# Kernel tuning notes

Measured on AMD Instinct MI355X. Metric: run time of the kernel, lower is better.

Reference implementation:

```python
import jax, jax.numpy as jnp
import numpy as np

N = 100000   # nodes
E = 1600000  # edges
H = 150      # hidden_dim
G = 256      # num graphs in batch
L = 5        # num_layers
GATE_H = 200


def setup_inputs() -> dict:
    key = jax.random.key(0)
    ks = jax.random.split(key, 12)
    s = lambda k, shape, fan: jax.random.normal(k, shape, dtype=jnp.float32) / np.sqrt(fan)
    return {
        "x": jax.random.normal(ks[0], (N, H), dtype=jnp.float32),
        "edge_index": jax.random.randint(ks[1], (2, E), 0, N, dtype=jnp.int64),
        "batch": jnp.sort(jax.random.randint(ks[2], (N,), 0, G, dtype=jnp.int64)),
        "W": s(ks[3], (L, H, H), H),              # GatedGraphConv per-layer weight
        "w_ih": s(ks[4], (3 * H, H), H),           # GRUCell input weights (r,z,n)
        "w_hh": s(ks[5], (3 * H, H), H),
        "b_ih": jnp.zeros((3 * H,), jnp.float32),
        "b_hh": jnp.zeros((3 * H,), jnp.float32),
        "gw1": s(ks[6], (H, GATE_H), H),           # gate_nn Linear(150,200)
        "gb1": jnp.zeros((GATE_H,), jnp.float32),
        "gw2": s(ks[7], (GATE_H, 1), GATE_H),      # gate_nn Linear(200,1)
        "gb2": jnp.zeros((1,), jnp.float32),
    }


def _gru_cell(m, h, w_ih, w_hh, b_ih, b_hh):
    gi = m @ w_ih.T + b_ih   # [N, 3H]
    gh = h @ w_hh.T + b_hh
    ir, iz, inn = jnp.split(gi, 3, axis=-1)
    hr, hz, hn = jnp.split(gh, 3, axis=-1)
    r = jax.nn.sigmoid(ir + hr)
    z = jax.nn.sigmoid(iz + hz)
    n = jnp.tanh(inn + r * hn)
    return (1.0 - z) * n + z * h


def reference(x, edge_index, batch, W, w_ih, w_hh, b_ih, b_hh, gw1, gb1, gw2, gb2):
    src, dst = edge_index[0], edge_index[1]
    h = x
    # GatedGraphConv: per layer, linear transform, scatter_add aggregation, GRU update
    for i in range(L):
        m = h @ W[i]                                   # [N, H]
        agg = jax.ops.segment_sum(m[src], dst, num_segments=N)  # scatter_add over edges
        h = _gru_cell(agg, h, w_ih, w_hh, b_ih, b_hh)
    # GlobalAttention readout
    gate = jnp.tanh(h @ gw1 + gb1) @ gw2 + gb2          # [N, 1]
    gmax = jax.ops.segment_max(gate, batch, num_segments=G)    # [G, 1]
    gate = jnp.exp(gate - gmax[batch])
    gsum = jax.ops.segment_sum(gate, batch, num_segments=G)    # [G, 1]
    gate = gate / (gsum[batch] + 1e-16)                 # segment softmax
    out = jax.ops.segment_sum(gate * h, batch, num_segments=G)  # [G, H]
    return out, gate
```

## Files before the change

kernel.cpp:

```cpp
#include <hip/hip_runtime.h>
#include <math.h>

#define NN 100000
#define NE 1600000
#define H 150
#define NG 256
#define NL 5
#define GH 200
#define HS 160
#define LS 168
#define CHN 1563
#define CH2 782
#define SNB 98
#define CSRMAX 2304000
#define NB 196
#define EBLK 782

typedef unsigned short u16;
typedef unsigned int   u32;
typedef __attribute__((ext_vector_type(8))) short bf16x8;
typedef __attribute__((ext_vector_type(4))) float f32x4;

__device__ __forceinline__ float bf2f(u32 lo16){ u32 t = lo16 << 16; return __builtin_bit_cast(float, t); }
__device__ __forceinline__ u16 f2bf(float f){
  u32 u = __builtin_bit_cast(u32, f);
  u += 0x7fffu + ((u >> 16) & 1u);
  return (u16)(u >> 16);
}
__device__ __forceinline__ u32 pack2(float a, float b){ return (u32)f2bf(a) | ((u32)f2bf(b) << 16); }
__device__ __forceinline__ float fast_sig(float x){
  float e = __expf(-x);
  return __builtin_amdgcn_rcpf(1.f + e);
}
__device__ __forceinline__ float fast_tanh(float x){
  float cx = fminf(fmaxf(x, -15.f), 15.f);
  float e = __expf(2.f*cx);
  return (e - 1.f) * __builtin_amdgcn_rcpf(e + 1.f);
}

__global__ void k_hist(const int* __restrict__ ed, int* __restrict__ cnt){
  int e = blockIdx.x*256 + threadIdx.x;
  if (e < NE) atomicAdd(&cnt[ed[e]], 1);
}

__global__ __launch_bounds__(256) void k_scan1(const int* __restrict__ cnt, int* __restrict__ part){
  __shared__ int red[256];
  const int b = blockIdx.x, tid = threadIdx.x;
  const int base = b*1024;
  int s = 0;
  #pragma unroll
  for (int i = 0; i < 4; ++i){
    int idx = base + tid + i*256;
    int v = (idx < NN) ? cnt[idx] : 0;
    s += (v + 7) & ~7;
  }
  red[tid] = s; __syncthreads();
  for (int st = 128; st >= 1; st >>= 1){
    if (tid < st) red[tid] += red[tid+st];
    __syncthreads();
  }
  if (tid == 0) part[b] = red[0];
}

__global__ void k_scan2(int* __restrict__ part){
  const int t = threadIdx.x;
  int v0 = (2*t   < SNB) ? part[2*t]   : 0;
  int v1 = (2*t+1 < SNB) ? part[2*t+1] : 0;
  int s = v0 + v1, x = s;
  #pragma unroll
  for (int off = 1; off < 64; off <<= 1){
    int tt = __shfl_up(x, off);
    if (t >= off) x += tt;
  }
  int excl = x - s;
  if (2*t   < SNB) part[2*t]   = excl;
  if (2*t+1 < SNB) part[2*t+1] = excl + v0;
}

__global__ __launch_bounds__(1024) void k_scan3(const int* __restrict__ cnt,
        const int* __restrict__ part, int* __restrict__ rowptr, int* __restrict__ cursor){
  __shared__ int wsum[16];
  const int b = blockIdx.x, tid = threadIdx.x;
  const int wid = tid >> 6, lane = tid & 63;
  const int idx = b*1024 + tid;
  int c = (idx < NN) ? cnt[idx] : 0;
  int v = (c + 7) & ~7;
  int x = v;
  #pragma unroll
  for (int off = 1; off < 64; off <<= 1){
    int t = __shfl_up(x, off);
    if (lane >= off) x += t;
  }
  if (lane == 63) wsum[wid] = x;
  __syncthreads();
  if (tid < 16){
    int s = wsum[tid];
    int y = s;
    #pragma unroll
    for (int off = 1; off < 16; off <<= 1){
      int t = __shfl_up(y, off);
      if (tid >= off) y += t;
    }
    wsum[tid] = y - s;
  }
  __syncthreads();
  if (idx < NN){
    int incl = part[b] + wsum[wid] + x;
    rowptr[idx+1] = incl;
    cursor[idx]   = incl - v;
  }
  if (idx == 0) rowptr[0] = 0;
}

__global__ __launch_bounds__(256) void k_pre(int* __restrict__ csr){
  int i = (blockIdx.x*256 + threadIdx.x)*4;
  int4 v = {NN, NN, NN, NN};
  *(int4*)&csr[i] = v;
}

__global__ __launch_bounds__(256) void k_bhist(const int* __restrict__ ed, int* __restrict__ bcnt){
  __shared__ int bh[NB];
  const int tid = threadIdx.x;
  for (int i = tid; i < NB; i += 256) bh[i] = 0;
  __syncthreads();
  const int base = blockIdx.x*2048;
  #pragma unroll
  for (int i = 0; i < 8; ++i){
    int e = base + i*256 + tid;
    if (e < NE) atomicAdd(&bh[ed[e] >> 9], 1);
  }
  __syncthreads();
  for (int i = tid; i < NB; i += 256) if (bh[i]) atomicAdd(&bcnt[i], bh[i]);
}

__global__ void k_bscan(const int* __restrict__ bcnt, int* __restrict__ bcur){
  __shared__ int ws[4];
  const int t = threadIdx.x, lane = t & 63, w = t >> 6;
  int v = (t < NB) ? bcnt[t] : 0;
  int x = v;
  #pragma unroll
  for (int off = 1; off < 64; off <<= 1){
    int tt = __shfl_up(x, off);
    if (lane >= off) x += tt;
  }
  if (lane == 63) ws[w] = x;
  __syncthreads();
  if (t == 0){
    int s = 0;
    #pragma unroll
    for (int i = 0; i < 4; ++i){ int tmp = ws[i]; ws[i] = s; s += tmp; }
  }
  __syncthreads();
  if (t < NB) bcur[t] = ws[w] + x - v;
}

__global__ __launch_bounds__(256) void k_bscatter(const int* __restrict__ es,
        const int* __restrict__ ed, int* __restrict__ bcur, int2* __restrict__ ebuf){
  __shared__ int lh[NB];
  __shared__ int lbase[NB];
  const int tid = threadIdx.x;
  for (int i = tid; i < NB; i += 256) lh[i] = 0;
  __syncthreads();
  const int base = blockIdx.x*2048;
  u32 meta[8]; int srcs[8], dsts[8];
  #pragma unroll
  for (int i = 0; i < 8; ++i){
    int e = base + i*256 + tid;
    if (e < NE){
      int d = ed[e];
      int b = d >> 9;
      int lr = atomicAdd(&lh[b], 1);
      meta[i] = ((u32)b << 16) | (u32)lr;
      srcs[i] = es[e]; dsts[i] = d;
    } else meta[i] = 0xffffffffu;
  }
  __syncthreads();
  for (int i = tid; i < NB; i += 256){
    int c = lh[i];
    lbase[i] = c ? atomicAdd(&bcur[i], c) : 0;
  }
  __syncthreads();
  #pragma unroll
  for (int i = 0; i < 8; ++i){
    if (meta[i] != 0xffffffffu){
      int b = meta[i] >> 16, lr = meta[i] & 0xffff;
      ebuf[lbase[b] + lr] = make_int2(srcs[i], dsts[i]);
    }
  }
}

__global__ void k_fill2(const int2* __restrict__ ebuf, int* __restrict__ cursor,
                        int* __restrict__ csr){
  int e = blockIdx.x*256 + threadIdx.x;
  if (e < NE){
    int2 sd = ebuf[e];
    int pos = atomicAdd(&cursor[sd.y], 1);
    csr[pos] = sd.x;
  }
}

__global__ __launch_bounds__(256) void k_wc(const float* __restrict__ W,
        const float* __restrict__ wih, float* __restrict__ Wc){
  int idx = blockIdx.x*256 + threadIdx.x;
  if (idx >= NL*H*450) return;
  int l = idx / (H*450);
  int rem = idx - l*H*450;
  int k = rem / 450;
  int j = rem - k*450;
  const float* Wr = W   + (size_t)l*H*H + (size_t)k*H;
  const float* wr = wih + (size_t)j*H;
  float acc = 0.f;
  for (int t = 0; t < H; ++t) acc = fmaf(Wr[t], wr[t], acc);
  Wc[idx] = acc;
}

__global__ void k_packi(const float* __restrict__ Wc, short* __restrict__ wbi){
  int idx = blockIdx.x*256 + threadIdx.x;
  int li = idx & 511;
  int q = idx >> 9;
  int mat = q % 3; q /= 3;
  int ks = q % 5;  q /= 5;
  int ct = q % 10; int l = q / 10;
  int lane = li >> 3, j = li & 7;
  int k = ks*32 + ((lane >> 4) << 3) + j;
  int col = ct*16 + (lane & 15);
  float v = (k < H && col < H) ? Wc[(size_t)l*H*450 + (size_t)k*450 + mat*H + col] : 0.f;
  wbi[idx] = (short)f2bf(v);
}

__global__ void k_packh(const float* __restrict__ whh, short* __restrict__ wbh){
  int idx = blockIdx.x*256 + threadIdx.x;
  int li = idx & 511;
  int q = idx >> 9;
  int mat = q % 3; q /= 3;
  int ks = q % 5;  int ct = q / 5;
  int lane = li >> 3, j = li & 7;
  int k = ks*32 + ((lane >> 4) << 3) + j;
  int col = ct*16 + (lane & 15);
  float v = (k < H && col < H) ? whh[(size_t)(mat*H + col)*H + k] : 0.f;
  wbh[idx] = (short)f2bf(v);
}

__global__ void k_packg(const float* __restrict__ gw1, short* __restrict__ gw1b){
  int idx = blockIdx.x*256 + threadIdx.x;
  int li = idx & 511;
  int q = idx >> 9;
  int ks = q % 5;  int ct = q / 5;
  int lane = li >> 3, j = li & 7;
  int k = ks*32 + ((lane >> 4) << 3) + j;
  int col = ct*16 + (lane & 15);
  float v = (k < H && col < GH) ? gw1[(size_t)k*GH + col] : 0.f;
  gw1b[idx] = (short)f2bf(v);
}

__global__ void k_cvt(const float* __restrict__ x, short* __restrict__ hb){
  int idx = blockIdx.x*256 + threadIdx.x;
  if (idx >= NN*80) return;
  int n = idx / 80, c2 = idx - n*80;
  int c = c2*2;
  float lo = (c   < H) ? x[(size_t)n*H + c]   : 0.f;
  float hi = (c+1 < H) ? x[(size_t)n*H + c+1] : 0.f;
  ((u32*)hb)[idx] = (u32)f2bf(lo) | ((u32)f2bf(hi) << 16);
}

__global__ void k_zrow(short* __restrict__ a, short* __restrict__ b){
  int t = threadIdx.x;
  if (t < 80){
    ((u32*)a)[(size_t)NN*80 + t] = 0u;
    ((u32*)b)[(size_t)NN*80 + t] = 0u;
  }
}

__global__ __launch_bounds__(256) void k_gather(const short* __restrict__ hb,
        const int* __restrict__ rowptr, const int* __restrict__ csr,
        short* __restrict__ aggb){
  const int lane = threadIdx.x & 63;
  const int n = blockIdx.x*4 + (threadIdx.x >> 6);
  if (n >= NN) return;
  const int s0 = rowptr[n], s1 = rowptr[n+1];
  const u32* h32 = (const u32*)hb;
  const bool ext = lane < 16;
  float x0=0.f, x1=0.f, y0=0.f, y1=0.f;
  for (int j = s0; j < s1; j += 8){
    int4 ia = *(const int4*)&csr[j];
    int4 ib = *(const int4*)&csr[j+4];
    const u32* r0 = h32 + (size_t)ia.x*80;
    const u32* r1 = h32 + (size_t)ia.y*80;
    const u32* r2 = h32 + (size_t)ia.z*80;
    const u32* r3 = h32 + (size_t)ia.w*80;
    const u32* r4 = h32 + (size_t)ib.x*80;
    const u32* r5 = h32 + (size_t)ib.y*80;
    const u32* r6 = h32 + (size_t)ib.z*80;
    const u32* r7 = h32 + (size_t)ib.w*80;
    u32 v0 = r0[lane], v1 = r1[lane], v2 = r2[lane], v3 = r3[lane];
    u32 v4 = r4[lane], v5 = r5[lane], v6 = r6[lane], v7 = r7[lane];
    u32 u0=0,u1=0,u2=0,u3=0,u4=0,u5=0,u6=0,u7=0;
    if (ext){
      u0 = r0[64+lane]; u1 = r1[64+lane]; u2 = r2[64+lane]; u3 = r3[64+lane];
      u4 = r4[64+lane]; u5 = r5[64+lane]; u6 = r6[64+lane]; u7 = r7[64+lane];
    }
    x0 += bf2f(v0 & 0xffffu) + bf2f(v1 & 0xffffu) + bf2f(v2 & 0xffffu) + bf2f(v3 & 0xffffu)
        + bf2f(v4 & 0xffffu) + bf2f(v5 & 0xffffu) + bf2f(v6 & 0xffffu) + bf2f(v7 & 0xffffu);
    x1 += bf2f(v0 >> 16) + bf2f(v1 >> 16) + bf2f(v2 >> 16) + bf2f(v3 >> 16)
        + bf2f(v4 >> 16) + bf2f(v5 >> 16) + bf2f(v6 >> 16) + bf2f(v7 >> 16);
    if (ext){
      y0 += bf2f(u0 & 0xffffu) + bf2f(u1 & 0xffffu) + bf2f(u2 & 0xffffu) + bf2f(u3 & 0xffffu)
          + bf2f(u4 & 0xffffu) + bf2f(u5 & 0xffffu) + bf2f(u6 & 0xffffu) + bf2f(u7 & 0xffffu);
      y1 += bf2f(u0 >> 16) + bf2f(u1 >> 16) + bf2f(u2 >> 16) + bf2f(u3 >> 16)
          + bf2f(u4 >> 16) + bf2f(u5 >> 16) + bf2f(u6 >> 16) + bf2f(u7 >> 16);
    }
  }
  u32* o = (u32*)aggb + (size_t)n*80;
  o[lane] = pack2(x0, x1);
  if (ext) o[64+lane] = pack2(y0, y1);
}

__global__ __launch_bounds__(256, 2) void k_gru(
    const short* __restrict__ aggb, const short* __restrict__ hbc,
    short* __restrict__ hbn,
    const short* __restrict__ wbi_l, const short* __restrict__ wbh,
    const float* __restrict__ bih, const float* __restrict__ bhh){
  __shared__ short sB[2][15360];
  const int tid = threadIdx.x;
  const int w = tid >> 6, lane = tid & 63;
  const int l16 = lane & 15, g = lane >> 4, g8 = g*8;
  const int row0 = blockIdx.x*128 + w*32;

  bf16x8 fA[2][5], fH[2][5];
  #pragma unroll
  for (int t = 0; t < 2; ++t){
    const int r = row0 + t*16 + l16;
    const bool rv = r < NN;
    #pragma unroll
    for (int ks = 0; ks < 5; ++ks){
      bf16x8 va = {0,0,0,0,0,0,0,0}, vh = {0,0,0,0,0,0,0,0};
      if (rv){
        va = *(const bf16x8*)&aggb[(size_t)r*HS + ks*32 + g8];
        vh = *(const bf16x8*)&hbc [(size_t)r*HS + ks*32 + g8];
      }
      fA[t][ks] = va; fH[t][ks] = vh;
    }
  }

  bf16x8 pr[8];
  #pragma unroll
  for (int k2 = 0; k2 < 8; ++k2){
    int u = tid + k2*256;
    if (u < 1920){
      int s = u >> 6, e = u & 63;
      const short* src = (s < 15) ? (wbi_l + s*512 + e*8)
                                  : (wbh  + (s-15)*512 + e*8);
      pr[k2] = *(const bf16x8*)src;
    }
  }
  #pragma unroll
  for (int k2 = 0; k2 < 8; ++k2){
    int u = tid + k2*256;
    if (u < 1920) *(bf16x8*)&sB[0][u*8] = pr[k2];
  }

  for (int ct = 0; ct < 10; ++ct){
    const int cur = ct & 1;
    __syncthreads();
    if (ct < 9){
      const int cto = (ct+1)*7680;
      #pragma unroll
      for (int k2 = 0; k2 < 8; ++k2){
        int u = tid + k2*256;
        if (u < 1920){
          int s = u >> 6, e = u & 63;
          const short* src = (s < 15) ? (wbi_l + cto + s*512 + e*8)
                                      : (wbh  + cto + (s-15)*512 + e*8);
          pr[k2] = *(const bf16x8*)src;
        }
      }
    }

    const int col = ct*16 + l16;
    const bool cv = col < H;
    const float bir = cv ? bih[col] : 0.f, biz = cv ? bih[H+col] : 0.f, bin_ = cv ? bih[2*H+col] : 0.f;
    const float bhr = cv ? bhh[col] : 0.f, bhz = cv ? bhh[H+col] : 0.f, bhn  = cv ? bhh[2*H+col] : 0.f;

    f32x4 ai[2][3], ah[2][3];
    #pragma unroll
    for (int t = 0; t < 2; ++t)
      #pragma unroll
      for (int m = 0; m < 3; ++m){ ai[t][m] = (f32x4){0,0,0,0}; ah[t][m] = (f32x4){0,0,0,0}; }

    const short* sbc = sB[cur];
    #pragma unroll
    for (int ks = 0; ks < 5; ++ks){
      bf16x8 bi0 = *(const bf16x8*)&sbc[(ks*3+0)*512 + lane*8];
      bf16x8 bi1 = *(const bf16x8*)&sbc[(ks*3+1)*512 + lane*8];
      bf16x8 bi2 = *(const bf16x8*)&sbc[(ks*3+2)*512 + lane*8];
      bf16x8 bh0 = *(const bf16x8*)&sbc[(15+ks*3+0)*512 + lane*8];
      bf16x8 bh1 = *(const bf16x8*)&sbc[(15+ks*3+1)*512 + lane*8];
      bf16x8 bh2 = *(const bf16x8*)&sbc[(15+ks*3+2)*512 + lane*8];
      #pragma unroll
      for (int t = 0; t < 2; ++t){
        ai[t][0] = __builtin_amdgcn_mfma_f32_16x16x32_bf16(fA[t][ks], bi0, ai[t][0], 0,0,0);
        ai[t][1] = __builtin_amdgcn_mfma_f32_16x16x32_bf16(fA[t][ks], bi1, ai[t][1], 0,0,0);
        ai[t][2] = __builtin_amdgcn_mfma_f32_16x16x32_bf16(fA[t][ks], bi2, ai[t][2], 0,0,0);
        ah[t][0] = __builtin_amdgcn_mfma_f32_16x16x32_bf16(fH[t][ks], bh0, ah[t][0], 0,0,0);
        ah[t][1] = __builtin_amdgcn_mfma_f32_16x16x32_bf16(fH[t][ks], bh1, ah[t][1], 0,0,0);
        ah[t][2] = __builtin_amdgcn_mfma_f32_16x16x32_bf16(fH[t][ks], bh2, ah[t][2], 0,0,0);
      }
    }

    if (ct < 9){
      #pragma unroll
      for (int k2 = 0; k2 < 8; ++k2){
        int u = tid + k2*256;
        if (u < 1920) *(bf16x8*)&sB[cur^1][u*8] = pr[k2];
      }
    }

    if (cv){
      #pragma unroll
      for (int t = 0; t < 2; ++t){
        #pragma unroll
        for (int r = 0; r < 4; ++r){
          int grow = row0 + t*16 + g*4 + r;
          if (grow < NN){
            float rr = fast_sig(ai[t][0][r]+bir + ah[t][0][r]+bhr);
            float zz = fast_sig(ai[t][1][r]+biz + ah[t][1][r]+bhz);
            float nn = fast_tanh(ai[t][2][r]+bin_ + rr*(ah[t][2][r]+bhn));
            float hold = bf2f((u32)(u16)hbc[(size_t)grow*HS + col]);
            float hnew = (1.f-zz)*nn + zz*hold;
            hbn[(size_t)grow*HS + col] = (short)f2bf(hnew);
          }
        }
      }
    }
  }
}

__global__ __launch_bounds__(256) void k_gatepre(const short* __restrict__ hb,
      const short* __restrict__ gw1b, const float* __restrict__ gb1,
      const float* __restrict__ gw2, const float* __restrict__ gb2,
      float* __restrict__ gbuf){
  __shared__ short sh[64*LS];
  __shared__ float part[4][4][4][4];
  const int tid = threadIdx.x;
  const int w = tid >> 6, lane = tid & 63;
  const int l16 = lane & 15, g = lane >> 4, g8 = g*8;
  const int chunk = blockIdx.x, row0 = chunk*64;

  for (int i = tid; i < 64*20; i += 256){
    int r = i/20, c = i - r*20;
    int gr = row0 + r;
    bf16x8 v = {0,0,0,0,0,0,0,0};
    if (gr < NN) v = *(const bf16x8*)&hb[(size_t)gr*HS + c*8];
    *(bf16x8*)&sh[r*LS + c*8] = v;
  }
  __syncthreads();

  float acc[4][4];
  #pragma unroll
  for (int rt=0; rt<4; ++rt){
    #pragma unroll
    for (int r=0; r<4; ++r) acc[rt][r] = 0.f;
  }
  for (int ct = w; ct < 13; ct += 4){
    bf16x8 B[5];
    const short* p = gw1b + (size_t)(ct*5)*512 + lane*8;
    #pragma unroll
    for (int ks = 0; ks < 5; ++ks) B[ks] = *(const bf16x8*)&p[ks*512];
    int col = ct*16 + l16;
    bool cv = col < GH;
    float g2 = cv ? gw2[col] : 0.f;
    float b1 = cv ? gb1[col] : 0.f;
    #pragma unroll
    for (int rt = 0; rt < 4; ++rt){
      f32x4 d = {0,0,0,0};
      #pragma unroll
      for (int ks = 0; ks < 5; ++ks){
        bf16x8 aH = *(const bf16x8*)&sh[(rt*16 + l16)*LS + ks*32 + g8];
        d = __builtin_amdgcn_mfma_f32_16x16x32_bf16(aH, B[ks], d, 0,0,0);
      }
      if (cv){
        #pragma unroll
        for (int r = 0; r < 4; ++r) acc[rt][r] += fast_tanh(d[r] + b1) * g2;
      }
    }
  }
  #pragma unroll
  for (int rt = 0; rt < 4; ++rt){
    #pragma unroll
    for (int r = 0; r < 4; ++r){
      float v = acc[rt][r];
      v += __shfl_xor(v, 1); v += __shfl_xor(v, 2);
      v += __shfl_xor(v, 4); v += __shfl_xor(v, 8);
      if (l16 == 0) part[w][rt][g][r] = v;
    }
  }
  __syncthreads();
  if (tid < 64){
    int rt = tid >> 4, gg = (tid >> 2) & 3, r = tid & 3;
    int grow = row0 + tid;
    if (grow < NN)
      gbuf[grow] = part[0][rt][gg][r] + part[1][rt][gg][r]
                 + part[2][rt][gg][r] + part[3][rt][gg][r] + gb2[0];
  }
}

__global__ __launch_bounds__(512) void k_readout(float* __restrict__ gatebuf,
    const short* __restrict__ hb, const int* __restrict__ batch,
    float* __restrict__ out, float* __restrict__ gate_out){
  const int g = blockIdx.x;
  const int tid = threadIdx.x;
  int lo=0, hi=NN;
  while (lo<hi){ int mid=(lo+hi)>>1; if (batch[mid] < g) lo=mid+1; else hi=mid; }
  const int start = lo;
  hi = NN;
  while (lo<hi){ int mid=(lo+hi)>>1; if (batch[mid] < g+1) lo=mid+1; else hi=mid; }
  const int end = lo;

  __shared__ float red[512];
  __shared__ float pacc[6][80][2];
  __shared__ float s_max, s_inv;
  float mx = -INFINITY;
  for (int n = start+tid; n < end; n += 512) mx = fmaxf(mx, gatebuf[n]);
  red[tid]=mx; __syncthreads();
  for (int s=256; s>=1; s>>=1){ if (tid<s) red[tid]=fmaxf(red[tid],red[tid+s]); __syncthreads(); }
  if (tid==0) s_max = red[0];
  __syncthreads();
  const float gmax = s_max;
  float sum = 0.f;
  for (int n = start+tid; n < end; n += 512){
    float e = expf(gatebuf[n]-gmax);
    gatebuf[n] = e;
    sum += e;
  }
  red[tid]=sum; __syncthreads();
  for (int s=256; s>=1; s>>=1){ if (tid<s) red[tid]+=red[tid+s]; __syncthreads(); }
  if (tid==0) s_inv = 1.0f/(red[0] + 1e-16f);
  __syncthreads();
  const float inv = s_inv;
  for (int n = start+tid; n < end; n += 512) gate_out[n] = gatebuf[n]*inv;

  const int col = tid % 80;
  const int grp = tid / 80;
  const u32* h32 = (const u32*)hb;
  if (grp < 6){
    float a0 = 0.f, a1 = 0.f;
    for (int n = start + grp; n < end; n += 6){
      u32 v = h32[(size_t)n*80 + col];
      float gv = gatebuf[n];
      a0 = fmaf(gv, bf2f(v & 0xffffu), a0);
      a1 = fmaf(gv, bf2f(v >> 16),     a1);
    }
    pacc[grp][col][0] = a0;
    pacc[grp][col][1] = a1;
  }
  __syncthreads();
  if (tid < 80){
    float a0 = 0.f, a1 = 0.f;
    #pragma unroll
    for (int q = 0; q < 6; ++q){ a0 += pacc[q][tid][0]; a1 += pacc[q][tid][1]; }
    int c0 = 2*tid, c1 = 2*tid + 1;
    if (c0 < H) out[g*H + c0] = a0*inv;
    if (c1 < H) out[g*H + c1] = a1*inv;
  }
}

extern "C" void kernel_launch(void* const* d_in, const int* in_sizes, int n_in,
                              void* d_out, int out_size, void* d_ws, size_t ws_size,
                              hipStream_t stream) {
  (void)in_sizes; (void)n_in; (void)out_size; (void)ws_size;
  const float* x    = (const float*)d_in[0];
  const int*   eidx = (const int*)d_in[1];
  const int*   batch= (const int*)d_in[2];
  const float* W    = (const float*)d_in[3];
  const float* wih  = (const float*)d_in[4];
  const float* whh  = (const float*)d_in[5];
  const float* bih  = (const float*)d_in[6];
  const float* bhh  = (const float*)d_in[7];
  const float* gw1  = (const float*)d_in[8];
  const float* gb1  = (const float*)d_in[9];
  const float* gw2  = (const float*)d_in[10];
  const float* gb2  = (const float*)d_in[11];

  float* out      = (float*)d_out;
  float* gate_out = out + NG*H;

  char* p = (char*)d_ws;
  float* gbuf  = (float*)p;  p += (size_t)NN*4;
  float* Wc    = (float*)p;  p += (size_t)NL*H*450*4;
  short* hb0   = (short*)p;  p += (size_t)(NN+1)*HS*2;
  short* hb1   = (short*)p;  p += (size_t)(NN+1)*HS*2;
  short* aggb  = (short*)p;  p += (size_t)NN*HS*2;
  short* wbi   = (short*)p;  p += (size_t)NL*76800*2;
  short* wbh   = (short*)p;  p += (size_t)76800*2;
  short* gw1b  = (short*)p;  p += (size_t)33280*2;
  int*   cnt   = (int*)p;    p += (size_t)NN*4;
  int*   rowptr= (int*)p;    p += (size_t)(NN+1)*4;
  int*   cursor= (int*)p;    p += (size_t)NN*4;
  int*   csr   = (int*)p;    p += (size_t)CSRMAX*4;
  int*   spart = (int*)p;    p += (size_t)SNB*4;
  int*   bcnt  = (int*)p;    p += (size_t)NB*4;
  int*   bcur  = (int*)p;    p += (size_t)NB*4;
  int2*  ebuf  = (int2*)p;   p += (size_t)NE*8;

  const int* esrc = eidx;
  const int* edst = eidx + NE;

  hipMemsetAsync(cnt, 0, sizeof(int)*NN, stream);
  hipMemsetAsync(bcnt, 0, sizeof(int)*NB, stream);
  k_hist<<<(NE+255)/256, 256, 0, stream>>>(edst, cnt);
  k_scan1<<<SNB, 256, 0, stream>>>(cnt, spart);
  k_scan2<<<1, 64, 0, stream>>>(spart);
  k_scan3<<<SNB, 1024, 0, stream>>>(cnt, spart, rowptr, cursor);
  k_pre <<<CSRMAX/1024, 256, 0, stream>>>(csr);
  k_bhist<<<EBLK, 256, 0, stream>>>(edst, bcnt);
  k_bscan<<<1, 256, 0, stream>>>(bcnt, bcur);
  k_bscatter<<<EBLK, 256, 0, stream>>>(esrc, edst, bcur, ebuf);
  k_fill2<<<(NE+255)/256, 256, 0, stream>>>(ebuf, cursor, csr);

  k_wc   <<<(NL*H*450+255)/256, 256, 0, stream>>>(W, wih, Wc);
  k_packi<<<1500, 256, 0, stream>>>(Wc, wbi);
  k_packh<<<300,  256, 0, stream>>>(whh, wbh);
  k_packg<<<130,  256, 0, stream>>>(gw1, gw1b);

  k_cvt<<<(NN*80+255)/256, 256, 0, stream>>>(x, hb0);
  k_zrow<<<1, 128, 0, stream>>>(hb0, hb1);

  for (int l = 0; l < NL; ++l){
    short* cur  = (l & 1) ? hb1 : hb0;
    short* next = (l & 1) ? hb0 : hb1;
    k_gather<<<NN/4, 256, 0, stream>>>(cur, rowptr, csr, aggb);
    k_gru<<<CH2, 256, 0, stream>>>(aggb, cur, next,
                                   wbi + (size_t)l*76800, wbh, bih, bhh);
  }
  k_gatepre<<<CHN, 256, 0, stream>>>(hb1, gw1b, gb1, gw2, gb2, gbuf);
  k_readout<<<NG, 512, 0, stream>>>(gbuf, hb1, batch, out, gate_out);
}
```

Before: 1.145 ms.

## Gather from column-sliced hidden-state copies so each block touches one slice

```diff
diff --git a/kernel.cpp b/kernel.cpp
--- a/kernel.cpp
+++ b/kernel.cpp
@@ -15,6 +15,7 @@
 #define CSRMAX 2304000
 #define NB 196
 #define EBLK 782
+#define SLICE_U32 1000010
 
 typedef unsigned short u16;
 typedef unsigned int   u32;
@@ -253,71 +254,67 @@
   gw1b[idx] = (short)f2bf(v);
 }
 
-__global__ void k_cvt(const float* __restrict__ x, short* __restrict__ hb){
+__global__ void k_cvt(const float* __restrict__ x, short* __restrict__ hb,
+                      u32* __restrict__ hbs){
   int idx = blockIdx.x*256 + threadIdx.x;
   if (idx >= NN*80) return;
   int n = idx / 80, c2 = idx - n*80;
   int c = c2*2;
   float lo = (c   < H) ? x[(size_t)n*H + c]   : 0.f;
   float hi = (c+1 < H) ? x[(size_t)n*H + c+1] : 0.f;
-  ((u32*)hb)[idx] = (u32)f2bf(lo) | ((u32)f2bf(hi) << 16);
-}
-
-__global__ void k_zrow(short* __restrict__ a, short* __restrict__ b){
+  u32 packed = (u32)f2bf(lo) | ((u32)f2bf(hi) << 16);
+  ((u32*)hb)[idx] = packed;
+  int cs = c2 / 10, off = c2 - cs*10;
+  hbs[(size_t)cs*SLICE_U32 + (size_t)n*10 + off] = packed;
+}
+
+__global__ void k_zrow(short* __restrict__ a, short* __restrict__ b,
+                       u32* __restrict__ sa, u32* __restrict__ sb){
   int t = threadIdx.x;
   if (t < 80){
     ((u32*)a)[(size_t)NN*80 + t] = 0u;
     ((u32*)b)[(size_t)NN*80 + t] = 0u;
-  }
-}
-
-__global__ __launch_bounds__(256) void k_gather(const short* __restrict__ hb,
+    int cs = t/10, off = t - cs*10;
+    sa[(size_t)cs*SLICE_U32 + (size_t)NN*10 + off] = 0u;
+    sb[(size_t)cs*SLICE_U32 + (size_t)NN*10 + off] = 0u;
+  }
+}
+
+__global__ __launch_bounds__(256) void k_gather(const u32* __restrict__ hbs,
         const int* __restrict__ rowptr, const int* __restrict__ csr,
-        short* __restrict__ aggb){
-  const int lane = threadIdx.x & 63;
-  const int n = blockIdx.x*4 + (threadIdx.x >> 6);
+        u32* __restrict__ aggb32){
+  const int tid = threadIdx.x;
+  const int w = tid >> 6, lane = tid & 63;
+  const int c = blockIdx.x & 7;
+  const int n = (blockIdx.x >> 3)*4 + w;
   if (n >= NN) return;
-  const int s0 = rowptr[n], s1 = rowptr[n+1];
-  const u32* h32 = (const u32*)hb;
-  const bool ext = lane < 16;
-  float x0=0.f, x1=0.f, y0=0.f, y1=0.f;
-  for (int j = s0; j < s1; j += 8){
-    int4 ia = *(const int4*)&csr[j];
-    int4 ib = *(const int4*)&csr[j+4];
-    const u32* r0 = h32 + (size_t)ia.x*80;
-    const u32* r1 = h32 + (size_t)ia.y*80;
-    const u32* r2 = h32 + (size_t)ia.z*80;
-    const u32* r3 = h32 + (size_t)ia.w*80;
-    const u32* r4 = h32 + (size_t)ib.x*80;
-    const u32* r5 = h32 + (size_t)ib.y*80;
-    const u32* r6 = h32 + (size_t)ib.z*80;
-    const u32* r7 = h32 + (size_t)ib.w*80;
-    u32 v0 = r0[lane], v1 = r1[lane], v2 = r2[lane], v3 = r3[lane];
-    u32 v4 = r4[lane], v5 = r5[lane], v6 = r6[lane], v7 = r7[lane];
-    u32 u0=0,u1=0,u2=0,u3=0,u4=0,u5=0,u6=0,u7=0;
-    if (ext){
-      u0 = r0[64+lane]; u1 = r1[64+lane]; u2 = r2[64+lane]; u3 = r3[64+lane];
-      u4 = r4[64+lane]; u5 = r5[64+lane]; u6 = r6[64+lane]; u7 = r7[64+lane];
-    }
-    x0 += bf2f(v0 & 0xffffu) + bf2f(v1 & 0xffffu) + bf2f(v2 & 0xffffu) + bf2f(v3 & 0xffffu)
-        + bf2f(v4 & 0xffffu) + bf2f(v5 & 0xffffu) + bf2f(v6 & 0xffffu) + bf2f(v7 & 0xffffu);
-    x1 += bf2f(v0 >> 16) + bf2f(v1 >> 16) + bf2f(v2 >> 16) + bf2f(v3 >> 16)
-        + bf2f(v4 >> 16) + bf2f(v5 >> 16) + bf2f(v6 >> 16) + bf2f(v7 >> 16);
-    if (ext){
-      y0 += bf2f(u0 & 0xffffu) + bf2f(u1 & 0xffffu) + bf2f(u2 & 0xffffu) + bf2f(u3 & 0xffffu)
-          + bf2f(u4 & 0xffffu) + bf2f(u5 & 0xffffu) + bf2f(u6 & 0xffffu) + bf2f(u7 & 0xffffu);
-      y1 += bf2f(u0 >> 16) + bf2f(u1 >> 16) + bf2f(u2 >> 16) + bf2f(u3 >> 16)
-          + bf2f(u4 >> 16) + bf2f(u5 >> 16) + bf2f(u6 >> 16) + bf2f(u7 >> 16);
-    }
-  }
-  u32* o = (u32*)aggb + (size_t)n*80;
-  o[lane] = pack2(x0, x1);
-  if (ext) o[64+lane] = pack2(y0, y1);
+  const int s0 = __builtin_nontemporal_load(&rowptr[n]);
+  const int s1 = __builtin_nontemporal_load(&rowptr[n+1]);
+  const u32* base = hbs + (size_t)c*SLICE_U32;
+  const int e = lane / 10;
+  const int u = lane - e*10;
+  const bool act = lane < 60;
+  float a0 = 0.f, a1 = 0.f;
+  for (int j = s0; j < s1; j += 6){
+    int idx = NN;
+    if (act && (j + e) < s1) idx = __builtin_nontemporal_load(&csr[j + e]);
+    u32 v = act ? base[(size_t)idx*10 + u] : 0u;
+    a0 += bf2f(v & 0xffffu);
+    a1 += bf2f(v >> 16);
+  }
+  float t0 = __shfl(a0, lane+30), t1 = __shfl(a1, lane+30);
+  if (lane < 30){ a0 += t0; a1 += t1; }
+  t0 = __shfl(a0, lane+10); t1 = __shfl(a1, lane+10);
+  if (lane < 10){ a0 += t0; a1 += t1; }
+  t0 = __shfl(a0, lane+20); t1 = __shfl(a1, lane+20);
+  if (lane < 10){ a0 += t0; a1 += t1; }
+  if (lane < 10)
+    __builtin_nontemporal_store(pack2(a0, a1), &aggb32[(size_t)n*80 + c*10 + lane]);
 }
 
 __global__ __launch_bounds__(256, 2) void k_gru(
     const short* __restrict__ aggb, const short* __restrict__ hbc,
-    short* __restrict__ hbn,
+    short* __restrict__ hbn, short* __restrict__ hbsn,
     const short* __restrict__ wbi_l, const short* __restrict__ wbh,
     const float* __restrict__ bih, const float* __restrict__ bhh){
   __shared__ short sB[2][15360];
@@ -416,6 +413,8 @@
     }
 
     if (cv){
+      const int j0 = col >> 1;
+      const int cs = j0 / 10, off = j0 - cs*10;
       #pragma unroll
       for (int t = 0; t < 2; ++t){
         #pragma unroll
@@ -427,7 +426,9 @@
             float nn = fast_tanh(ai[t][2][r]+bin_ + rr*(ah[t][2][r]+bhn));
             float hold = bf2f((u32)(u16)hbc[(size_t)grow*HS + col]);
             float hnew = (1.f-zz)*nn + zz*hold;
-            hbn[(size_t)grow*HS + col] = (short)f2bf(hnew);
+            short hv = (short)f2bf(hnew);
+            hbn[(size_t)grow*HS + col] = hv;
+            hbsn[(size_t)cs*(2*(size_t)SLICE_U32) + (size_t)grow*20 + off*2 + (col & 1)] = hv;
           }
         }
       }
@@ -589,6 +590,8 @@
   float* Wc    = (float*)p;  p += (size_t)NL*H*450*4;
   short* hb0   = (short*)p;  p += (size_t)(NN+1)*HS*2;
   short* hb1   = (short*)p;  p += (size_t)(NN+1)*HS*2;
+  short* hbs0  = (short*)p;  p += (size_t)8*SLICE_U32*4;
+  short* hbs1  = (short*)p;  p += (size_t)8*SLICE_U32*4;
   short* aggb  = (short*)p;  p += (size_t)NN*HS*2;
   short* wbi   = (short*)p;  p += (size_t)NL*76800*2;
   short* wbh   = (short*)p;  p += (size_t)76800*2;
@@ -622,14 +625,16 @@
   k_packh<<<300,  256, 0, stream>>>(whh, wbh);
   k_packg<<<130,  256, 0, stream>>>(gw1, gw1b);
 
-  k_cvt<<<(NN*80+255)/256, 256, 0, stream>>>(x, hb0);
-  k_zrow<<<1, 128, 0, stream>>>(hb0, hb1);
+  k_cvt<<<(NN*80+255)/256, 256, 0, stream>>>(x, hb0, (u32*)hbs0);
+  k_zrow<<<1, 128, 0, stream>>>(hb0, hb1, (u32*)hbs0, (u32*)hbs1);
 
   for (int l = 0; l < NL; ++l){
-    short* cur  = (l & 1) ? hb1 : hb0;
-    short* next = (l & 1) ? hb0 : hb1;
-    k_gather<<<NN/4, 256, 0, stream>>>(cur, rowptr, csr, aggb);
-    k_gru<<<CH2, 256, 0, stream>>>(aggb, cur, next,
+    short* cur   = (l & 1) ? hb1 : hb0;
+    short* next  = (l & 1) ? hb0 : hb1;
+    short* curS  = (l & 1) ? hbs1 : hbs0;
+    short* nextS = (l & 1) ? hbs0 : hbs1;
+    k_gather<<<8*((NN+3)/4), 256, 0, stream>>>((const u32*)curS, rowptr, csr, (u32*)aggb);
+    k_gru<<<CH2, 256, 0, stream>>>(aggb, cur, next, nextS,
                                    wbi + (size_t)l*76800, wbh, bih, bhh);
   }
   k_gatepre<<<CHN, 256, 0, stream>>>(hb1, gw1b, gb1, gw2, gb2, gbuf);
```

Result: slower. 2.767 ms (+141.6%).
